# Kernel optimization log

Measured on AMD Instinct MI355X. Metric: run time of the kernel, lower is better.

The kernel has to match this reference:

```python
import jax, jax.numpy as jnp
import numpy as np

N_QUBITS = 8
N_QLAYERS = 2
D_MODEL = 8
NUM_HEADS = 2
DEPTH = D_MODEL // NUM_HEADS


def _apply_1q(state, U, wire):
    # state: (T, 2, 2, ..., 2); U: (2, 2) complex
    state = jnp.moveaxis(state, 1 + wire, -1)
    state = jnp.einsum('...b,ab->...a', state, U)
    return jnp.moveaxis(state, -1, 1 + wire)


def _apply_cnot(state, ctrl, tgt):
    s = jnp.moveaxis(state, (1 + ctrl, 1 + tgt), (-2, -1))
    s = jnp.concatenate([s[..., :1, :], s[..., 1:, ::-1]], axis=-2)
    return jnp.moveaxis(s, (-2, -1), (1 + ctrl, 1 + tgt))


def _z_signs(n):
    idx = jnp.arange(2 ** n)
    bits = (idx[:, None] >> jnp.arange(n - 1, -1, -1)[None, :]) & 1  # col i = qubit i
    return (1.0 - 2.0 * bits).astype(jnp.float32)  # (2^n, n)


def quantum_circuit(x, w):
    """AngleEmbedding(RX) + BasicEntanglerLayers(RX + CNOT ring) + PauliZ expvals.
    x: (T, n) float angles; w: (L, n) float weights -> (T, n) float expvals."""
    T, n = x.shape
    L = w.shape[0]
    # AngleEmbedding: RX(x_i)|0> = cos(x_i/2)|0> - i sin(x_i/2)|1>; product state
    h = 0.5 * x
    amps = jnp.stack([jnp.cos(h).astype(jnp.complex64),
                      (-1j) * jnp.sin(h).astype(jnp.complex64)], axis=-1)  # (T, n, 2)
    state = amps[:, 0, :]
    for i in range(1, n):
        state = (state[:, :, None] * amps[:, i, None, :]).reshape(T, -1)
    state = state.reshape((T,) + (2,) * n)
    for l in range(L):
        for i in range(n):
            th = 0.5 * w[l, i]
            cc = jnp.cos(th).astype(jnp.complex64)
            ss = (-1j) * jnp.sin(th).astype(jnp.complex64)
            U = jnp.stack([jnp.stack([cc, ss]), jnp.stack([ss, cc])])  # RX(w)
            state = _apply_1q(state, U, i)
        pairs = [(i, (i + 1) % n) for i in range(n)] if n > 2 else [(0, 1)]
        for c, t in pairs:
            state = _apply_cnot(state, c, t)
    probs = jnp.abs(state.reshape(T, -1)) ** 2  # (T, 2^n)
    return probs @ _z_signs(n)  # (T, n)


def setup_inputs() -> dict:
    key = jax.random.key(0)
    ks = jax.random.split(key, 8)
    B, S, d = 32, 1024, D_MODEL
    q = jax.random.normal(ks[0], (B, S, d), dtype=jnp.float32)
    k = jax.random.normal(ks[1], (B, S, d), dtype=jnp.float32)
    v = jax.random.normal(ks[2], (B, S, d), dtype=jnp.float32)
    mask = jnp.triu(jnp.ones((S, S), dtype=jnp.float32), k=1)[None, None]  # causal
    weights_q = jax.random.uniform(ks[3], (N_QLAYERS, N_QUBITS), dtype=jnp.float32, maxval=2 * np.pi)
    weights_k = jax.random.uniform(ks[4], (N_QLAYERS, N_QUBITS), dtype=jnp.float32, maxval=2 * np.pi)
    weights_v = jax.random.uniform(ks[5], (N_QLAYERS, N_QUBITS), dtype=jnp.float32, maxval=2 * np.pi)
    weights_dense = jax.random.uniform(ks[6], (N_QLAYERS, N_QUBITS), dtype=jnp.float32, maxval=2 * np.pi)
    return {"q": q, "k": k, "v": v, "mask": mask,
            "weights_q": weights_q, "weights_k": weights_k,
            "weights_v": weights_v, "weights_dense": weights_dense}


def reference(q, k, v, mask, weights_q, weights_k, weights_v, weights_dense):
    B, S, d = q.shape
    T = B * S
    # per-token quantum Q/K/V embeddings (batched over all B*S tokens)
    qe = quantum_circuit(q.reshape(T, d), weights_q).reshape(B, S, d)
    ke = quantum_circuit(k.reshape(T, d), weights_k).reshape(B, S, d)
    ve = quantum_circuit(v.reshape(T, d), weights_v).reshape(B, S, d)
    # split heads: (B, H, S, depth)
    def split(x):
        return x.reshape(B, S, NUM_HEADS, DEPTH).transpose(0, 2, 1, 3)
    qh, kh, vh = split(qe), split(ke), split(ve)
    scores = jnp.einsum('bhqd,bhkd->bhqk', qh, kh) / jnp.sqrt(jnp.float32(DEPTH))
    scores = scores + mask * (-1e9)
    attn = jax.nn.softmax(scores, axis=-1)
    ctx = jnp.einsum('bhqk,bhkd->bhqd', attn, vh)
    ctx = ctx.transpose(0, 2, 1, 3).reshape(B, S, d)
    out = quantum_circuit(ctx.reshape(T, d), weights_dense).reshape(B, S, d)
    return out, attn
```

## Files before the change

kernel.cpp:

```cpp
#include <hip/hip_runtime.h>

#define S_LEN 1024
#define BATCH 32
#define NHEAD 2
#define HDIM  4


#define TBL_STRIDE 256

__global__ __launch_bounds__(256)
void pauli_setup(const float* __restrict__ wq, const float* __restrict__ wk,
                 const float* __restrict__ wv, const float* __restrict__ wd,
                 float4* __restrict__ tables, int* __restrict__ counts)
{
    int blk = blockIdx.x;
    int set = blk >> 3, w = blk & 7;
    const float* wt = (set == 0) ? wq : (set == 1) ? wk : (set == 2) ? wv : wd;

    float c2[8], s2[8];
#pragma unroll
    for (int j = 0; j < 8; ++j) {
        float th = wt[8 + j];
        s2[j] = __sinf(th);
        c2[j] = __cosf(th);
    }

    unsigned X = 0u, Z = 1u << w;
    int sg0 = 0;
#pragma unroll
    for (int g = 7; g >= 0; --g) {
        int c = g, t = (g + 1) & 7;
        unsigned xc = (X >> c) & 1u, zt = (Z >> t) & 1u;
        unsigned xt = (X >> t) & 1u, zc = (Z >> c) & 1u;
        sg0 ^= (int)(xc & zt & (xt ^ zc ^ 1u));
        X ^= xc << t;
        Z ^= zt << c;
    }

    int tid = threadIdx.x;
    float coef = sg0 ? -1.0f : 1.0f;
    unsigned Xb = X;
    int k = 0;
#pragma unroll
    for (int j = 0; j < 8; ++j) {
        if ((Z >> j) & 1u) {
            int bit = (tid >> k) & 1;
            ++k;
            if (!((X >> j) & 1u)) {
                if (bit) { Xb |= 1u << j; coef *= s2[j]; }
                else     { coef *= c2[j]; }
            } else {
                if (bit) { Xb &= ~(1u << j); coef *= -s2[j]; }
                else     { coef *= c2[j]; }
            }
        }
    }
    bool valid = (tid < (1 << k));

    unsigned Xf = Xb, Zf = Z;
    int sg = 0;
#pragma unroll
    for (int g = 7; g >= 0; --g) {
        int c = g, t = (g + 1) & 7;
        unsigned xc = (Xf >> c) & 1u, zt = (Zf >> t) & 1u;
        unsigned xt = (Xf >> t) & 1u, zc = (Zf >> c) & 1u;
        sg ^= (int)(xc & zt & (xt ^ zc ^ 1u));
        Xf ^= xc << t;
        Zf ^= zt << c;
    }

    bool keep = valid && ((Xf & ~Zf) == 0u);
    if (sg ^ (__popc(Xf) & 1)) coef = -coef;
    unsigned zonly = Zf & ~Xf;
    unsigned ymask = Xf;

    __shared__ int wsum[4];
    int lane = tid & 63, wvx = tid >> 6;
    unsigned long long mb = __ballot((int)keep);
    if (lane == 0) wsum[wvx] = __popcll(mb);
    __syncthreads();
    int prefix = 0;
#pragma unroll
    for (int i = 0; i < 4; ++i)
        if (i < wvx) prefix += wsum[i];
    int pos = prefix + __popcll(mb & ((1ull << lane) - 1ull));
    if (keep) {
        float4 t4;
        t4.x = __int_as_float((int)zonly);
        t4.y = __int_as_float((int)ymask);
        t4.z = coef;
        t4.w = 0.0f;
        tables[blk * TBL_STRIDE + pos] = t4;
    }
    __syncthreads();
    if (tid == 0) counts[blk] = wsum[0] + wsum[1] + wsum[2] + wsum[3];
}

__global__ __launch_bounds__(256)
void qc_eval(const float* __restrict__ x0, const float* __restrict__ w0a,
             const float* __restrict__ x1, const float* __restrict__ w0b,
             const float* __restrict__ x2, const float* __restrict__ w0c,
             const float4* __restrict__ tables, const int* __restrict__ counts,
             float* __restrict__ o0, float* __restrict__ o1, float* __restrict__ o2,
             int rows_per_seg, int set_base)
{
    int gr = blockIdx.x * 256 + threadIdx.x;
    int seg = gr / rows_per_seg;
    int row = gr - seg * rows_per_seg;
    const float* x  = (seg == 0) ? x0 : (seg == 1) ? x1 : x2;
    const float* w0 = (seg == 0) ? w0a : (seg == 1) ? w0b : w0c;
    float*       o  = (seg == 0) ? o0 : (seg == 1) ? o1 : o2;
    int set = set_base + seg;

    const float4* xp = reinterpret_cast<const float4*>(x + (size_t)row * 8);
    float4 xa = xp[0], xb = xp[1];
    float cc[8], ss[8];
    {
        float a;
        a = xa.x + w0[0]; __sincosf(a, &ss[0], &cc[0]);
        a = xa.y + w0[1]; __sincosf(a, &ss[1], &cc[1]);
        a = xa.z + w0[2]; __sincosf(a, &ss[2], &cc[2]);
        a = xa.w + w0[3]; __sincosf(a, &ss[3], &cc[3]);
        a = xb.x + w0[4]; __sincosf(a, &ss[4], &cc[4]);
        a = xb.y + w0[5]; __sincosf(a, &ss[5], &cc[5]);
        a = xb.z + w0[6]; __sincosf(a, &ss[6], &cc[6]);
        a = xb.w + w0[7]; __sincosf(a, &ss[7], &cc[7]);
    }

    float res[8];
#pragma unroll
    for (int w = 0; w < 8; ++w) {
        int blk = set * 8 + w;
        int cnt = counts[blk];
        const float4* base = tables + blk * TBL_STRIDE;
        float acc = 0.0f;
        for (int t = 0; t < cnt; ++t) {
            float4 T = base[t];
            unsigned zm = (unsigned)__float_as_int(T.x);
            unsigned ym = (unsigned)__float_as_int(T.y);
            float v = T.z;
#pragma unroll
            for (int m = 0; m < 8; ++m) {
                float f = ((ym >> m) & 1u) ? ss[m]
                        : (((zm >> m) & 1u) ? cc[m] : 1.0f);
                v *= f;
            }
            acc += v;
        }
        res[w] = acc;
    }

    float4* op = reinterpret_cast<float4*>(o + (size_t)row * 8);
    op[0] = make_float4(res[0], res[1], res[2], res[3]);
    op[1] = make_float4(res[4], res[5], res[6], res[7]);
}

template <int CTRL>
__device__ __forceinline__ float dpp_add(float x)
{
    int xi = __float_as_int(x);
    int yi = __builtin_amdgcn_update_dpp(xi, xi, CTRL, 0xf, 0xf, false);
    return x + __int_as_float(yi);
}

__device__ __forceinline__ float wave_allsum(float x)
{
    x = dpp_add<0xB1>(x);
    x = dpp_add<0x4E>(x);
    x = dpp_add<0x124>(x);
    x = dpp_add<0x128>(x);
    x += __shfl_xor(x, 16);
    x += __shfl_xor(x, 32);
    return x;
}

__global__ __launch_bounds__(256)
void attn_kernel(const float* qe, const float* __restrict__ ke,
                 const float* __restrict__ ve, float* __restrict__ attn,
                 float* ctx)
{
    __shared__ float4 kT[S_LEN];
    __shared__ float4 vT[S_LEN];

    int tid = threadIdx.x;
    int bid = blockIdx.x;
    int it  = bid & 15;
    int h   = (bid >> 4) & 1;
    int b   = bid >> 5;
    int lane = tid & 63;
    int wave = tid >> 6;

    const float4* ke4 = reinterpret_cast<const float4*>(ke) + h;
    const float4* ve4 = reinterpret_cast<const float4*>(ve) + h;
    size_t rowbase = (size_t)b * S_LEN;

    for (int j = tid; j < S_LEN; j += 256) {
        kT[j] = ke4[(rowbase + j) * 2];
        vT[j] = ve4[(rowbase + j) * 2];
    }
    __syncthreads();

    int i0 = it * 64 + wave * 16;
    const float* qp = qe + (rowbase + i0) * 8 + h * HDIM;

    for (int pr = 0; pr < 8; ++pr) {
        int i = i0 + pr * 2;
        float4 qa = *reinterpret_cast<const float4*>(qp + pr * 16);
        float4 qb = *reinterpret_cast<const float4*>(qp + pr * 16 + 8);
        qa.x *= 0.5f; qa.y *= 0.5f; qa.z *= 0.5f; qa.w *= 0.5f;
        qb.x *= 0.5f; qb.y *= 0.5f; qb.z *= 0.5f; qb.w *= 0.5f;

        float pe0[16], pe1[16];
        float sum0 = 0.0f, sum1 = 0.0f;
        float a0 = 0, a1 = 0, a2 = 0, a3 = 0;
        float c0 = 0, c1 = 0, c2 = 0, c3 = 0;
#pragma unroll
        for (int t = 0; t < 16; ++t) {
            int j = t * 64 + lane;
            float4 kk = kT[j];
            float4 vv = vT[j];
            float s0 = qa.x * kk.x + qa.y * kk.y + qa.z * kk.z + qa.w * kk.w;
            float s1 = qb.x * kk.x + qb.y * kk.y + qb.z * kk.z + qb.w * kk.w;
            float p0 = (j <= i)     ? __expf(s0) : 0.0f;
            float p1 = (j <= i + 1) ? __expf(s1) : 0.0f;
            pe0[t] = p0; pe1[t] = p1;
            sum0 += p0; sum1 += p1;
            a0 += p0 * vv.x; a1 += p0 * vv.y; a2 += p0 * vv.z; a3 += p0 * vv.w;
            c0 += p1 * vv.x; c1 += p1 * vv.y; c2 += p1 * vv.z; c3 += p1 * vv.w;
        }
        sum0 = wave_allsum(sum0);
        sum1 = wave_allsum(sum1);
        float inv0 = 1.0f / sum0;
        float inv1 = 1.0f / sum1;

        size_t base0 = (((size_t)(b * NHEAD + h)) * S_LEN + i) * S_LEN;
#pragma unroll
        for (int t = 0; t < 16; ++t) {
            __builtin_nontemporal_store(pe0[t] * inv0, &attn[base0 + t * 64 + lane]);
            __builtin_nontemporal_store(pe1[t] * inv1, &attn[base0 + S_LEN + t * 64 + lane]);
        }

        a0 = wave_allsum(a0); a1 = wave_allsum(a1);
        a2 = wave_allsum(a2); a3 = wave_allsum(a3);
        c0 = wave_allsum(c0); c1 = wave_allsum(c1);
        c2 = wave_allsum(c2); c3 = wave_allsum(c3);
        if (lane == 0) {
            float* cp = ctx + (rowbase + i) * 8 + h * HDIM;
            cp[0] = a0 * inv0; cp[1] = a1 * inv0;
            cp[2] = a2 * inv0; cp[3] = a3 * inv0;
            cp[8] = c0 * inv1; cp[9] = c1 * inv1;
            cp[10] = c2 * inv1; cp[11] = c3 * inv1;
        }
    }
}

extern "C" void kernel_launch(void* const* d_in, const int* in_sizes, int n_in,
                              void* d_out, int out_size, void* d_ws, size_t ws_size,
                              hipStream_t stream)
{
    const float* q  = (const float*)d_in[0];
    const float* k  = (const float*)d_in[1];
    const float* v  = (const float*)d_in[2];
    const float* wq = (const float*)d_in[4];
    const float* wk = (const float*)d_in[5];
    const float* wv = (const float*)d_in[6];
    const float* wd = (const float*)d_in[7];

    float* out  = (float*)d_out;
    float* attn = out + (size_t)BATCH * S_LEN * 8;

    float*  ws     = (float*)d_ws;
    float*  qe     = ws;
    float*  ke     = ws + 262144;
    float*  ve     = ws + 524288;
    float4* tables = (float4*)(ws + 786432);
    int*    counts = (int*)(ws + 786432 + 32768);

    const int rows = BATCH * S_LEN;

    pauli_setup<<<dim3(32), 256, 0, stream>>>(wq, wk, wv, wd, tables, counts);

    qc_eval<<<dim3(rows * 3 / 256), 256, 0, stream>>>(
        q, wq, k, wk, v, wv, tables, counts, qe, ke, ve, rows, 0);

    attn_kernel<<<dim3(BATCH * NHEAD * 16), 256, 0, stream>>>(qe, ke, ve, attn, qe);

    qc_eval<<<dim3(rows / 256), 256, 0, stream>>>(
        qe, wd, qe, wd, qe, wd, tables, counts, out, out, out, rows, 3);
}
```

Baseline: 95.37 us.

## Store attention rows as float4 and use DPP row-shift reductions in attn kernel

Reorganizes K/V in shared memory into four interleaved columns so each lane handles four consecutive key positions. Attention probabilities can then be written as float4 vector stores instead of scalar nontemporal stores. The wave all-reduce (DPP plus two cross-lane shuffles) is replaced by a DPP row_shr/row_bcast reduction into lane 63 followed by a readlane broadcast. The nontemporal hint on the large attn output is dropped, which may change cache behaviour for the dominant write traffic.

```diff
diff --git a/kernel.cpp b/kernel.cpp
--- a/kernel.cpp
+++ b/kernel.cpp
@@ -156,22 +156,26 @@
 }
 
 template <int CTRL>
-__device__ __forceinline__ float dpp_add(float x)
-{
-    int xi = __float_as_int(x);
-    int yi = __builtin_amdgcn_update_dpp(xi, xi, CTRL, 0xf, 0xf, false);
-    return x + __int_as_float(yi);
-}
-
-__device__ __forceinline__ float wave_allsum(float x)
-{
-    x = dpp_add<0xB1>(x);
-    x = dpp_add<0x4E>(x);
-    x = dpp_add<0x124>(x);
-    x = dpp_add<0x128>(x);
-    x += __shfl_xor(x, 16);
-    x += __shfl_xor(x, 32);
+__device__ __forceinline__ float dpp_acc(float x)
+{
+    int y = __builtin_amdgcn_update_dpp(0, __float_as_int(x), CTRL, 0xf, 0xf, false);
+    return x + __int_as_float(y);
+}
+
+__device__ __forceinline__ float wave_reduce63(float x)
+{
+    x = dpp_acc<0x111>(x);
+    x = dpp_acc<0x112>(x);
+    x = dpp_acc<0x114>(x);
+    x = dpp_acc<0x118>(x);
+    x = dpp_acc<0x142>(x);
+    x = dpp_acc<0x143>(x);
     return x;
+}
+
+__device__ __forceinline__ float bcast63(float x)
+{
+    return __int_as_float(__builtin_amdgcn_readlane(__float_as_int(x), 63));
 }
 
 __global__ __launch_bounds__(256)
@@ -179,8 +183,8 @@
                  const float* __restrict__ ve, float* __restrict__ attn,
                  float* ctx)
 {
-    __shared__ float4 kT[S_LEN];
-    __shared__ float4 vT[S_LEN];
+    __shared__ float4 kc[4][S_LEN / 4];
+    __shared__ float4 vc[4][S_LEN / 4];
 
     int tid = threadIdx.x;
     int bid = blockIdx.x;
@@ -195,61 +199,77 @@
     size_t rowbase = (size_t)b * S_LEN;
 
     for (int j = tid; j < S_LEN; j += 256) {
-        kT[j] = ke4[(rowbase + j) * 2];
-        vT[j] = ve4[(rowbase + j) * 2];
+        kc[j & 3][j >> 2] = ke4[(rowbase + j) * 2];
+        vc[j & 3][j >> 2] = ve4[(rowbase + j) * 2];
     }
     __syncthreads();
 
     int i0 = it * 64 + wave * 16;
     const float* qp = qe + (rowbase + i0) * 8 + h * HDIM;
+    float4* attn4 = reinterpret_cast<float4*>(attn);
+    size_t head4 = ((size_t)(b * NHEAD + h)) * S_LEN * (S_LEN / 4);
 
     for (int pr = 0; pr < 8; ++pr) {
         int i = i0 + pr * 2;
+
         float4 qa = *reinterpret_cast<const float4*>(qp + pr * 16);
         float4 qb = *reinterpret_cast<const float4*>(qp + pr * 16 + 8);
         qa.x *= 0.5f; qa.y *= 0.5f; qa.z *= 0.5f; qa.w *= 0.5f;
         qb.x *= 0.5f; qb.y *= 0.5f; qb.z *= 0.5f; qb.w *= 0.5f;
 
-        float pe0[16], pe1[16];
-        float sum0 = 0.0f, sum1 = 0.0f;
-        float a0 = 0, a1 = 0, a2 = 0, a3 = 0;
-        float c0 = 0, c1 = 0, c2 = 0, c3 = 0;
-#pragma unroll
-        for (int t = 0; t < 16; ++t) {
-            int j = t * 64 + lane;
-            float4 kk = kT[j];
-            float4 vv = vT[j];
-            float s0 = qa.x * kk.x + qa.y * kk.y + qa.z * kk.z + qa.w * kk.w;
-            float s1 = qb.x * kk.x + qb.y * kk.y + qb.z * kk.z + qb.w * kk.w;
-            float p0 = (j <= i)     ? __expf(s0) : 0.0f;
-            float p1 = (j <= i + 1) ? __expf(s1) : 0.0f;
-            pe0[t] = p0; pe1[t] = p1;
-            sum0 += p0; sum1 += p1;
-            a0 += p0 * vv.x; a1 += p0 * vv.y; a2 += p0 * vv.z; a3 += p0 * vv.w;
-            c0 += p1 * vv.x; c1 += p1 * vv.y; c2 += p1 * vv.z; c3 += p1 * vv.w;
-        }
-        sum0 = wave_allsum(sum0);
-        sum1 = wave_allsum(sum1);
-        float inv0 = 1.0f / sum0;
-        float inv1 = 1.0f / sum1;
-
-        size_t base0 = (((size_t)(b * NHEAD + h)) * S_LEN + i) * S_LEN;
-#pragma unroll
-        for (int t = 0; t < 16; ++t) {
-            __builtin_nontemporal_store(pe0[t] * inv0, &attn[base0 + t * 64 + lane]);
-            __builtin_nontemporal_store(pe1[t] * inv1, &attn[base0 + S_LEN + t * 64 + lane]);
-        }
-
-        a0 = wave_allsum(a0); a1 = wave_allsum(a1);
-        a2 = wave_allsum(a2); a3 = wave_allsum(a3);
-        c0 = wave_allsum(c0); c1 = wave_allsum(c1);
-        c2 = wave_allsum(c2); c3 = wave_allsum(c3);
-        if (lane == 0) {
+        float pea[16], peb[16];
+        float suma = 0.0f, sumb = 0.0f;
+        float4 pva = {0, 0, 0, 0}, pvb = {0, 0, 0, 0};
+
+#pragma unroll
+        for (int t = 0; t < 4; ++t) {
+            int m = t * 64 + lane;
+            int jb = m << 2;
+#pragma unroll
+            for (int c = 0; c < 4; ++c) {
+                float4 kk = kc[c][m];
+                float4 vv = vc[c][m];
+                float sa = qa.x * kk.x + qa.y * kk.y + qa.z * kk.z + qa.w * kk.w;
+                float sb = qb.x * kk.x + qb.y * kk.y + qb.z * kk.z + qb.w * kk.w;
+                int j = jb + c;
+                float pa = (j <= i)     ? __expf(sa) : 0.0f;
+                float pb = (j <= i + 1) ? __expf(sb) : 0.0f;
+                pea[t * 4 + c] = pa;
+                peb[t * 4 + c] = pb;
+                suma += pa; sumb += pb;
+                pva.x += pa * vv.x; pva.y += pa * vv.y;
+                pva.z += pa * vv.z; pva.w += pa * vv.w;
+                pvb.x += pb * vv.x; pvb.y += pb * vv.y;
+                pvb.z += pb * vv.z; pvb.w += pb * vv.w;
+            }
+        }
+
+        float inva = 1.0f / bcast63(wave_reduce63(suma));
+        float invb = 1.0f / bcast63(wave_reduce63(sumb));
+
+        size_t base4 = head4 + (size_t)i * (S_LEN / 4) + lane;
+#pragma unroll
+        for (int t = 0; t < 4; ++t) {
+            float4 oa, ob;
+            oa.x = pea[t * 4 + 0] * inva; oa.y = pea[t * 4 + 1] * inva;
+            oa.z = pea[t * 4 + 2] * inva; oa.w = pea[t * 4 + 3] * inva;
+            ob.x = peb[t * 4 + 0] * invb; ob.y = peb[t * 4 + 1] * invb;
+            ob.z = peb[t * 4 + 2] * invb; ob.w = peb[t * 4 + 3] * invb;
+            attn4[base4 + t * 64] = oa;
+            attn4[base4 + (S_LEN / 4) + t * 64] = ob;
+        }
+
+        pva.x = wave_reduce63(pva.x); pva.y = wave_reduce63(pva.y);
+        pva.z = wave_reduce63(pva.z); pva.w = wave_reduce63(pva.w);
+        pvb.x = wave_reduce63(pvb.x); pvb.y = wave_reduce63(pvb.y);
+        pvb.z = wave_reduce63(pvb.z); pvb.w = wave_reduce63(pvb.w);
+
+        if (lane == 63) {
             float* cp = ctx + (rowbase + i) * 8 + h * HDIM;
-            cp[0] = a0 * inv0; cp[1] = a1 * inv0;
-            cp[2] = a2 * inv0; cp[3] = a3 * inv0;
-            cp[8] = c0 * inv1; cp[9] = c1 * inv1;
-            cp[10] = c2 * inv1; cp[11] = c3 * inv1;
+            cp[0]  = pva.x * inva; cp[1]  = pva.y * inva;
+            cp[2]  = pva.z * inva; cp[3]  = pva.w * inva;
+            cp[8]  = pvb.x * invb; cp[9]  = pvb.y * invb;
+            cp[10] = pvb.z * invb; cp[11] = pvb.w * invb;
         }
     }
 }
```

Measured after the change: 91.42 us. 1.04x faster.
